# Optimization experiments

Measured on AMD Instinct MI355X. Metric: run time of the kernel, lower is better.

Reference implementation:

```python
import jax, jax.numpy as jnp
import numpy as np

N_NODES = 50000
MAX_NODES = 50000
POS_DIM = 64
IN_DIM = 128
HID = 64
N_LAYERS = 3
BN_EPS = 1e-5


def sinusoidal_encoding(max_len, d_model):
    position = jnp.arange(max_len, dtype=jnp.float32)[:, None]
    div_term = jnp.exp(jnp.arange(0, d_model, 2, dtype=jnp.float32) * (-np.log(10000.0) / d_model))
    ang = position * div_term  # [max_len, d_model//2]
    # interleave sin (even cols) and cos (odd cols)
    return jnp.stack([jnp.sin(ang), jnp.cos(ang)], axis=-1).reshape(max_len, d_model)


def batch_norm(h, gamma, beta):
    mean = jnp.mean(h, axis=0)
    var = jnp.mean(jnp.square(h - mean), axis=0)  # biased, as torch BN training
    return (h - mean) * jax.lax.rsqrt(var + BN_EPS) * gamma + beta


def gcn_conv(h, W, b, row, col, ew, n):
    # PyG GCNConv: h' = D^-1/2 (A + I) D^-1/2 (h W) + b, self-loop weight 1
    hw = h @ W  # [N, HID]
    deg = jnp.zeros((n,), h.dtype).at[col].add(ew) + 1.0  # +1 for self loop
    dinv = jax.lax.rsqrt(deg)
    norm = dinv[row] * ew * dinv[col]  # [E]
    agg = jax.ops.segment_sum(norm[:, None] * hw[row], col, num_segments=n)
    agg = agg + (dinv * dinv)[:, None] * hw  # self-loop term
    return agg + b


def setup_inputs():
    key = jax.random.key(0)
    ks = jax.random.split(key, 16)
    E = 800000
    inp = {
        'x': jax.random.normal(ks[0], (N_NODES, IN_DIM), dtype=jnp.float32),
        'edge_index': jax.random.randint(ks[1], (2, E), 0, N_NODES, dtype=jnp.int32),
        'edge_weight': jax.random.uniform(ks[2], (E,), dtype=jnp.float32),
        'positions': jnp.arange(N_NODES, dtype=jnp.int32),
        'ft_W': jax.random.normal(ks[3], (IN_DIM + POS_DIM, HID), dtype=jnp.float32) * 0.05,
        'ft_b': jnp.zeros((HID,), jnp.float32),
        'ft_gamma': jnp.ones((HID,), jnp.float32),
        'ft_beta': jnp.zeros((HID,), jnp.float32),
        'conv_W': jax.random.normal(ks[4], (N_LAYERS, HID, HID), dtype=jnp.float32) * 0.1,
        'conv_b': jnp.zeros((N_LAYERS, HID), jnp.float32),
        'bn_gamma': jnp.ones((N_LAYERS, HID), jnp.float32),
        'bn_beta': jnp.zeros((N_LAYERS, HID), jnp.float32),
        'out_W1': jax.random.normal(ks[5], (HID, HID // 2), dtype=jnp.float32) * 0.1,
        'out_b1': jnp.zeros((HID // 2,), jnp.float32),
        'out_W2': jax.random.normal(ks[6], (HID // 2, 1), dtype=jnp.float32) * 0.1,
        'out_b2': jnp.zeros((1,), jnp.float32),
    }
    return inp


def reference(x, edge_index, edge_weight, positions, ft_W, ft_b, ft_gamma, ft_beta,
              conv_W, conv_b, bn_gamma, bn_beta, out_W1, out_b1, out_W2, out_b2):
    n = x.shape[0]
    row, col = edge_index[0], edge_index[1]
    pe = sinusoidal_encoding(MAX_NODES, POS_DIM)
    h = jnp.concatenate([x, pe[positions]], axis=1)
    # feature_transform: Linear -> BN -> ReLU (dropout = identity in eval)
    h = jax.nn.relu(batch_norm(h @ ft_W + ft_b, ft_gamma, ft_beta))
    for i in range(N_LAYERS):
        identity = h
        h = gcn_conv(h, conv_W[i], conv_b[i], row, col, edge_weight, n)
        h = jax.nn.relu(batch_norm(h, bn_gamma[i], bn_beta[i]))
        h = h + identity
    h = jax.nn.relu(h @ out_W1 + out_b1)
    out = h @ out_W2 + out_b2  # [N, 1]
    return out.squeeze()
```

## Files before the change

### kernel.cpp

```cpp
#include <hip/hip_runtime.h>
#include <hip/hip_fp16.h>
#include <math.h>

#define HID 64
#define IN_DIM 128
#define POS_DIM 64
#define FT_IN 192
#define BN_EPS 1e-5f
#define PAD 68
#define MAXDEG 64

static inline size_t align256(size_t x){ return (x + 255) & ~(size_t)255; }


__global__ void k_init(unsigned long long* bins, float* statsAll, int N){
  int i = blockIdx.x*blockDim.x + threadIdx.x;
  if (i < N) bins[i] = 0ULL;
  if (i < 512) statsAll[i] = 0.f;
}

__global__ void k_build(const int* __restrict__ row, const int* __restrict__ col,
                        const float* __restrict__ ew,
                        unsigned long long* bins, unsigned* wedges, int E){
  int e = blockIdx.x*blockDim.x + threadIdx.x;
  if (e < E){
    int r = row[e], c = col[e];
    float w = ew[e];
    unsigned long long v = (1ULL<<40)
        | (unsigned long long)(unsigned)__float2uint_rn(w*16777216.0f);
    unsigned long long old = atomicAdd(&bins[c], v);
    unsigned q = (unsigned)(old >> 40);
    if (q < MAXDEG){
      __half hw16 = __float2half(w);
      wedges[(size_t)c*MAXDEG + q] =
          (unsigned)r | ((unsigned)*(unsigned short*)&hw16 << 16);
    }
  }
}

__global__ void k_dinv(const unsigned long long* __restrict__ bins,
                       float* dinv, int N){
  int i = blockIdx.x*blockDim.x + threadIdx.x;
  if (i < N){
    float deg = (float)(bins[i] & 0xFFFFFFFFFFULL) * 5.9604645e-8f;
    dinv[i] = rsqrtf(deg + 1.0f);
  }
}


#define MICRO_FMA(a, b, acc)                                   \
  acc[0].x = fmaf(a.x, b.x, acc[0].x);                         \
  acc[0].y = fmaf(a.x, b.y, acc[0].y);                         \
  acc[0].z = fmaf(a.x, b.z, acc[0].z);                         \
  acc[0].w = fmaf(a.x, b.w, acc[0].w);                         \
  acc[1].x = fmaf(a.y, b.x, acc[1].x);                         \
  acc[1].y = fmaf(a.y, b.y, acc[1].y);                         \
  acc[1].z = fmaf(a.y, b.z, acc[1].z);                         \
  acc[1].w = fmaf(a.y, b.w, acc[1].w);                         \
  acc[2].x = fmaf(a.z, b.x, acc[2].x);                         \
  acc[2].y = fmaf(a.z, b.y, acc[2].y);                         \
  acc[2].z = fmaf(a.z, b.z, acc[2].z);                         \
  acc[2].w = fmaf(a.z, b.w, acc[2].w);                         \
  acc[3].x = fmaf(a.w, b.x, acc[3].x);                         \
  acc[3].y = fmaf(a.w, b.y, acc[3].y);                         \
  acc[3].z = fmaf(a.w, b.z, acc[3].z);                         \
  acc[3].w = fmaf(a.w, b.w, acc[3].w);

__global__ __launch_bounds__(256) void k_h0(
    const float* __restrict__ x, const int* __restrict__ positions,
    const float* __restrict__ ftW, float* __restrict__ h0, float* stats, int N)
{
  __shared__ __align__(16) float Xs[32*PAD];
  __shared__ __align__(16) float Wc[32*64];
  __shared__ float redS[16*64];
  __shared__ float redQ[16*64];
  int tx = threadIdx.x;
  int n0 = blockIdx.x * 64;
  int c4 = (tx & 15) * 4;
  int r4 = (tx >> 4) * 4;
  float4 acc[4];
  acc[0] = acc[1] = acc[2] = acc[3] = make_float4(0.f,0.f,0.f,0.f);

  for (int kc = 0; kc < 6; ++kc){
    #pragma unroll
    for (int i = 0; i < 8; ++i)
      Wc[tx + i*256] = ftW[kc*2048 + tx + i*256];
    if (kc < 4){
      #pragma unroll
      for (int i = 0; i < 2; ++i){
        int s = tx + i*256;
        int row = s >> 3, kk = (s & 7) * 4;
        float4 v = make_float4(0.f,0.f,0.f,0.f);
        int n = n0 + row;
        if (n < N) v = *(const float4*)&x[(size_t)n*IN_DIM + kc*32 + kk];
        Xs[(kk+0)*PAD + row] = v.x;
        Xs[(kk+1)*PAD + row] = v.y;
        Xs[(kk+2)*PAD + row] = v.z;
        Xs[(kk+3)*PAD + row] = v.w;
      }
    } else {
      #pragma unroll
      for (int i = 0; i < 4; ++i){
        int s = tx + i*256;
        int m = s & 63, jj = s >> 6;
        int j = (kc-4)*16 + jj;
        int n = n0 + m;
        float sv = 0.f, cv = 0.f;
        if (n < N){
          float ang = (float)positions[n] * expf((float)(2*j) * -0.14391157f);
          sv = __sinf(ang); cv = __cosf(ang);
        }
        Xs[(2*jj+0)*PAD + m] = sv;
        Xs[(2*jj+1)*PAD + m] = cv;
      }
    }
    __syncthreads();
    #pragma unroll 8
    for (int k = 0; k < 32; ++k){
      float4 a = *(const float4*)(Xs + k*PAD + r4);
      float4 b = *(const float4*)(Wc + k*64 + c4);
      MICRO_FMA(a, b, acc);
    }
    __syncthreads();
  }

  float cs[4] = {0,0,0,0}, cq[4] = {0,0,0,0};
  #pragma unroll
  for (int i = 0; i < 4; ++i){
    int n = n0 + r4 + i;
    if (n < N) *(float4*)&h0[(size_t)n*HID + c4] = acc[i];
    float4 v = (n < N) ? acc[i] : make_float4(0,0,0,0);
    cs[0] += v.x; cs[1] += v.y; cs[2] += v.z; cs[3] += v.w;
    cq[0] += v.x*v.x; cq[1] += v.y*v.y; cq[2] += v.z*v.z; cq[3] += v.w*v.w;
  }
  int g = tx >> 4;
  #pragma unroll
  for (int j = 0; j < 4; ++j){
    redS[g*64 + c4 + j] = cs[j];
    redQ[g*64 + c4 + j] = cq[j];
  }
  __syncthreads();
  if (tx < 64){
    float s = 0.f, q = 0.f;
    #pragma unroll
    for (int gg = 0; gg < 16; ++gg){ s += redS[gg*64 + tx]; q += redQ[gg*64 + tx]; }
    atomicAdd(&stats[tx], s);
    atomicAdd(&stats[64+tx], q);
  }
}

__global__ __launch_bounds__(256) void k_layer(
    const float* __restrict__ aggb, const float* __restrict__ stats,
    const float* __restrict__ gamma, const float* __restrict__ beta, float invN,
    float* __restrict__ hbuf, const float* __restrict__ W,
    const float* __restrict__ dinv, __half* __restrict__ hwh, int N, int residual)
{
  __shared__ __align__(16) float Ws[64*64];
  __shared__ __align__(16) float Hs[64*PAD];
  __shared__ float coefS[128];
  int tx = threadIdx.x;
  int n0 = blockIdx.x * 64;
  if (tx < 64){
    float s = stats[tx], s2 = stats[64+tx];
    float mean = s * invN;
    float var = s2 * invN - mean*mean;
    float scale = rsqrtf(var + BN_EPS) * gamma[tx];
    coefS[tx] = scale;
    coefS[64+tx] = beta[tx] - mean*scale;
  }
  #pragma unroll
  for (int i = 0; i < 16; ++i) Ws[tx + i*256] = W[tx + i*256];
  __syncthreads();
  #pragma unroll
  for (int i = 0; i < 4; ++i){
    int s = tx + i*256;
    int row = s >> 4, cc = (s & 15) * 4;
    int n = n0 + row;
    float4 r = make_float4(0.f,0.f,0.f,0.f);
    if (n < N){
      float4 v = *(const float4*)&aggb[(size_t)n*HID + cc];
      r.x = fmaxf(fmaf(v.x, coefS[cc+0], coefS[64+cc+0]), 0.f);
      r.y = fmaxf(fmaf(v.y, coefS[cc+1], coefS[64+cc+1]), 0.f);
      r.z = fmaxf(fmaf(v.z, coefS[cc+2], coefS[64+cc+2]), 0.f);
      r.w = fmaxf(fmaf(v.w, coefS[cc+3], coefS[64+cc+3]), 0.f);
      if (residual){
        float4 o = *(const float4*)&hbuf[(size_t)n*HID + cc];
        r.x += o.x; r.y += o.y; r.z += o.z; r.w += o.w;
      }
      *(float4*)&hbuf[(size_t)n*HID + cc] = r;
    }
    Hs[(cc+0)*PAD + row] = r.x;
    Hs[(cc+1)*PAD + row] = r.y;
    Hs[(cc+2)*PAD + row] = r.z;
    Hs[(cc+3)*PAD + row] = r.w;
  }
  __syncthreads();
  int c4 = (tx & 15) * 4;
  int r4 = (tx >> 4) * 4;
  float4 acc[4];
  acc[0] = acc[1] = acc[2] = acc[3] = make_float4(0.f,0.f,0.f,0.f);
  #pragma unroll 8
  for (int k = 0; k < 64; ++k){
    float4 a = *(const float4*)(Hs + k*PAD + r4);
    float4 b = *(const float4*)(Ws + k*64 + c4);
    MICRO_FMA(a, b, acc);
  }
  #pragma unroll
  for (int i = 0; i < 4; ++i){
    int n = n0 + r4 + i;
    if (n < N){
      float dn = dinv[n];
      __half2 h01 = __floats2half2_rn(dn*acc[i].x, dn*acc[i].y);
      __half2 h23 = __floats2half2_rn(dn*acc[i].z, dn*acc[i].w);
      *(__half2*)&hwh[(size_t)n*HID + c4]     = h01;
      *(__half2*)&hwh[(size_t)n*HID + c4 + 2] = h23;
    }
  }
}

__global__ __launch_bounds__(256) void k_agg(
    const __half* __restrict__ hwh, const unsigned long long* __restrict__ bins,
    const unsigned* __restrict__ wedges, const float* __restrict__ dinv,
    float* __restrict__ agg, float* stats, int N)
{
  __shared__ float red[512];
  int tx = threadIdx.x;
  int k = tx & 63, w = tx >> 6;
  int n0 = blockIdx.x * 16;
  float ssum = 0.f, ssq = 0.f;
  for (int it = 0; it < 4; ++it){
    int n = n0 + w*4 + it;
    if (n < N){
      int cnt = (int)(bins[n] >> 40);
      if (cnt > MAXDEG) cnt = MAXDEG;
      float acc0 = __half2float(hwh[(size_t)n*HID + k]);
      float acc1 = 0.f, acc2 = 0.f, acc3 = 0.f;
      float acc4 = 0.f, acc5 = 0.f, acc6 = 0.f, acc7 = 0.f;
      unsigned md = (k < cnt) ? wedges[(size_t)n*MAXDEG + k] : 0u;
      int j = 0;
      #define EDGE(T, ACC) {                                              \
        unsigned m_ = __shfl(md, j + T, 64);                              \
        unsigned short eh_ = (unsigned short)(m_ >> 16);                  \
        float ww_ = __half2float(*(__half*)&eh_);                         \
        float g_ = __half2float(hwh[(size_t)(m_ & 0xFFFFu)*HID + k]);     \
        ACC = fmaf(ww_, g_, ACC); }
      for (; j + 8 <= cnt; j += 8){
        EDGE(0, acc0) EDGE(1, acc1) EDGE(2, acc2) EDGE(3, acc3)
        EDGE(4, acc4) EDGE(5, acc5) EDGE(6, acc6) EDGE(7, acc7)
      }
      for (; j < cnt; ++j){ EDGE(0, acc0) }
      #undef EDGE
      float total = ((acc0 + acc1) + (acc2 + acc3))
                  + ((acc4 + acc5) + (acc6 + acc7));
      total *= dinv[n];
      agg[(size_t)n*HID + k] = total;
      ssum += total; ssq += total*total;
    }
  }
  red[tx] = ssum; red[256+tx] = ssq;
  __syncthreads();
  if (tx < 64){
    float s  = red[tx]     + red[64+tx]  + red[128+tx] + red[192+tx];
    float s2 = red[256+tx] + red[320+tx] + red[384+tx] + red[448+tx];
    atomicAdd(&stats[tx], s);
    atomicAdd(&stats[64+tx], s2);
  }
}

__global__ __launch_bounds__(256) void k_out(
    const float* __restrict__ aggb, const float* __restrict__ stats,
    const float* __restrict__ gamma, const float* __restrict__ beta, float invN,
    const float* __restrict__ hbuf,
    const float* __restrict__ W1, const float* __restrict__ b1,
    const float* __restrict__ W2, const float* __restrict__ b2,
    float* __restrict__ out, int N)
{
  __shared__ __align__(16) float Hs[64*PAD];
  __shared__ float red[256];
  __shared__ float coefS[128];
  int tx = threadIdx.x;
  int n0 = blockIdx.x * 64;
  if (tx < 64){
    float s = stats[tx], s2 = stats[64+tx];
    float mean = s * invN;
    float var = s2 * invN - mean*mean;
    float scale = rsqrtf(var + BN_EPS) * gamma[tx];
    coefS[tx] = scale;
    coefS[64+tx] = beta[tx] - mean*scale;
  }
  __syncthreads();
  #pragma unroll
  for (int i = 0; i < 4; ++i){
    int s = tx + i*256;
    int row = s >> 4, cc = (s & 15) * 4;
    int n = n0 + row;
    float4 r = make_float4(0.f,0.f,0.f,0.f);
    if (n < N){
      float4 v = *(const float4*)&aggb[(size_t)n*HID + cc];
      r.x = fmaxf(fmaf(v.x, coefS[cc+0], coefS[64+cc+0]), 0.f);
      r.y = fmaxf(fmaf(v.y, coefS[cc+1], coefS[64+cc+1]), 0.f);
      r.z = fmaxf(fmaf(v.z, coefS[cc+2], coefS[64+cc+2]), 0.f);
      r.w = fmaxf(fmaf(v.w, coefS[cc+3], coefS[64+cc+3]), 0.f);
      float4 o = *(const float4*)&hbuf[(size_t)n*HID + cc];
      r.x += o.x; r.y += o.y; r.z += o.z; r.w += o.w;
    }
    Hs[(cc+0)*PAD + row] = r.x;
    Hs[(cc+1)*PAD + row] = r.y;
    Hs[(cc+2)*PAD + row] = r.z;
    Hs[(cc+3)*PAD + row] = r.w;
  }
  __syncthreads();
  int m = tx & 63, w = tx >> 6, j0 = w*8;
  float acc[8] = {0,0,0,0,0,0,0,0};
  #pragma unroll 8
  for (int k = 0; k < 64; ++k){
    float hv = Hs[k*PAD + m];
    #pragma unroll
    for (int j = 0; j < 8; ++j)
      acc[j] = fmaf(hv, W1[k*32 + j0 + j], acc[j]);
  }
  float part = 0.f;
  #pragma unroll
  for (int j = 0; j < 8; ++j)
    part += fmaxf(acc[j] + b1[j0+j], 0.f) * W2[j0+j];
  red[w*64 + m] = part;
  __syncthreads();
  if (tx < 64){
    int n = n0 + tx;
    if (n < N) out[n] = red[tx] + red[64+tx] + red[128+tx] + red[192+tx] + b2[0];
  }
}

extern "C" void kernel_launch(void* const* d_in, const int* in_sizes, int n_in,
                              void* d_out, int out_size, void* d_ws, size_t ws_size,
                              hipStream_t stream)
{
  const float* x         = (const float*)d_in[0];
  const int*   ei        = (const int*)d_in[1];
  const float* ew        = (const float*)d_in[2];
  const int*   positions = (const int*)d_in[3];
  const float* ftW       = (const float*)d_in[4];
  const float* ft_gamma  = (const float*)d_in[6];
  const float* ft_beta   = (const float*)d_in[7];
  const float* convW     = (const float*)d_in[8];
  const float* bn_gamma  = (const float*)d_in[10];
  const float* bn_beta   = (const float*)d_in[11];
  const float* outW1     = (const float*)d_in[12];
  const float* outb1     = (const float*)d_in[13];
  const float* outW2     = (const float*)d_in[14];
  const float* outb2     = (const float*)d_in[15];
  float* out = (float*)d_out;

  int N = in_sizes[0] / IN_DIM;
  int E = in_sizes[1] / 2;
  const int* row  = ei;
  const int* colv = ei + E;

  char* p = (char*)d_ws;
  auto alloc = [&](size_t bytes){ char* r = p; p += align256(bytes); return r; };
  unsigned long long* bins = (unsigned long long*)alloc((size_t)N*8);
  float*    dinv   = (float*)alloc((size_t)N*4);
  unsigned* wedges = (unsigned*)alloc((size_t)N*MAXDEG*4);
  __half*   hwh    = (__half*)alloc((size_t)N*HID*2);
  float*    aggb   = (float*)alloc((size_t)N*HID*4);
  float*    hbuf   = (float*)alloc((size_t)N*HID*4);
  float*    statsAll = (float*)alloc(512*4);

  float* stats0 = statsAll;
  float* stats1 = statsAll + 128;
  float* stats2 = statsAll + 256;
  float* stats3 = statsAll + 384;

  int nb_n  = (N+255)/256;
  int nb_e  = (E+255)/256;
  int nb64  = (N+63)/64;
  int nb16  = (N+15)/16;
  float invN = 1.0f/(float)N;

  k_init <<<nb_n,256,0,stream>>>(bins,statsAll,N);
  k_build<<<nb_e,256,0,stream>>>(row,colv,ew,bins,wedges,E);
  k_dinv <<<nb_n,256,0,stream>>>(bins,dinv,N);

  k_h0  <<<nb64,256,0,stream>>>(x,positions,ftW,aggb,stats0,N);

  float* statsIn[4] = {stats0, stats1, stats2, stats3};
  for (int i = 0; i < 3; ++i){
    const float* g = (i==0) ? ft_gamma : bn_gamma + (size_t)(i-1)*HID;
    const float* b = (i==0) ? ft_beta  : bn_beta  + (size_t)(i-1)*HID;
    k_layer<<<nb64,256,0,stream>>>(aggb,statsIn[i],g,b,invN,hbuf,
                                   convW + (size_t)i*HID*HID,dinv,hwh,N,(i>0)?1:0);
    k_agg  <<<nb16,256,0,stream>>>(hwh,bins,wedges,dinv,aggb,statsIn[i+1],N);
  }

  k_out<<<nb64,256,0,stream>>>(aggb,stats3,bn_gamma+2*HID,bn_beta+2*HID,invN,
                               hbuf,outW1,outb1,outW2,outb2,out,N);
}
```

Baseline: 437.7 us.

## Split fp16 features into column halves and aggregate each half separately

The transformed features are now stored as two separate N×32 half-precision arrays instead of one N×64 array, and the aggregation runs twice, once per half. Each 32-lane half-wavefront processes its own node. The intent is to shrink each gather pass's working set (3.2MB per half) so it fits better in cache and random neighbor gathers hit more often. The cost is reading the edge lists twice and launching an extra kernel per layer. Edge-list loads and output stores are marked nontemporal.

```diff
diff --git a/kernel.cpp b/kernel.cpp
--- a/kernel.cpp
+++ b/kernel.cpp
@@ -153,7 +153,8 @@
     const float* __restrict__ aggb, const float* __restrict__ stats,
     const float* __restrict__ gamma, const float* __restrict__ beta, float invN,
     float* __restrict__ hbuf, const float* __restrict__ W,
-    const float* __restrict__ dinv, __half* __restrict__ hwh, int N, int residual)
+    const float* __restrict__ dinv, __half* __restrict__ hwhA,
+    __half* __restrict__ hwhB, int N, int residual)
 {
   __shared__ __align__(16) float Ws[64*64];
   __shared__ __align__(16) float Hs[64*PAD];
@@ -212,58 +213,81 @@
       float dn = dinv[n];
       __half2 h01 = __floats2half2_rn(dn*acc[i].x, dn*acc[i].y);
       __half2 h23 = __floats2half2_rn(dn*acc[i].z, dn*acc[i].w);
-      *(__half2*)&hwh[(size_t)n*HID + c4]     = h01;
-      *(__half2*)&hwh[(size_t)n*HID + c4 + 2] = h23;
-    }
-  }
-}
-
-__global__ __launch_bounds__(256) void k_agg(
-    const __half* __restrict__ hwh, const unsigned long long* __restrict__ bins,
+      __half* dst = (c4 < 32) ? (hwhA + (size_t)n*32 + c4)
+                              : (hwhB + (size_t)n*32 + (c4 - 32));
+      *(__half2*)&dst[0] = h01;
+      *(__half2*)&dst[2] = h23;
+    }
+  }
+}
+
+__global__ __launch_bounds__(256) void k_aggH(
+    const __half* __restrict__ hwhH, const unsigned long long* __restrict__ bins,
     const unsigned* __restrict__ wedges, const float* __restrict__ dinv,
-    float* __restrict__ agg, float* stats, int N)
+    float* __restrict__ agg, float* stats, int N, int halfOff)
 {
-  __shared__ float red[512];
+  __shared__ float redS[8*32];
+  __shared__ float redQ[8*32];
   int tx = threadIdx.x;
-  int k = tx & 63, w = tx >> 6;
-  int n0 = blockIdx.x * 16;
-  float ssum = 0.f, ssq = 0.f;
-  for (int it = 0; it < 4; ++it){
-    int n = n0 + w*4 + it;
-    if (n < N){
-      int cnt = (int)(bins[n] >> 40);
-      if (cnt > MAXDEG) cnt = MAXDEG;
-      float acc0 = __half2float(hwh[(size_t)n*HID + k]);
-      float acc1 = 0.f, acc2 = 0.f, acc3 = 0.f;
-      float acc4 = 0.f, acc5 = 0.f, acc6 = 0.f, acc7 = 0.f;
-      unsigned md = (k < cnt) ? wedges[(size_t)n*MAXDEG + k] : 0u;
-      int j = 0;
-      #define EDGE(T, ACC) {                                              \
-        unsigned m_ = __shfl(md, j + T, 64);                              \
-        unsigned short eh_ = (unsigned short)(m_ >> 16);                  \
-        float ww_ = __half2float(*(__half*)&eh_);                         \
-        float g_ = __half2float(hwh[(size_t)(m_ & 0xFFFFu)*HID + k]);     \
-        ACC = fmaf(ww_, g_, ACC); }
-      for (; j + 8 <= cnt; j += 8){
-        EDGE(0, acc0) EDGE(1, acc1) EDGE(2, acc2) EDGE(3, acc3)
-        EDGE(4, acc4) EDGE(5, acc5) EDGE(6, acc6) EDGE(7, acc7)
+  int lane = tx & 63, w = tx >> 6;
+  int hs = lane >> 5;
+  int k = lane & 31;
+  float csum = 0.f, csq = 0.f;
+  int nbase = blockIdx.x*16 + w*4;
+  for (int it = 0; it < 2; ++it){
+    int n = nbase + it*2 + hs;
+    bool act = (n < N);
+    int nn = act ? n : 0;
+    int cnt = act ? (int)(bins[nn] >> 40) : 0;
+    if (cnt > MAXDEG) cnt = MAXDEG;
+    unsigned md0 = (k < cnt)
+        ? __builtin_nontemporal_load(&wedges[(size_t)nn*MAXDEG + k]) : 0u;
+    unsigned md1 = (32 + k < cnt)
+        ? __builtin_nontemporal_load(&wedges[(size_t)nn*MAXDEG + 32 + k]) : 0u;
+    int cm = cnt;
+    cm = max(cm, __shfl_xor(cm, 32, 64));
+    float a0 = act ? __half2float(hwhH[(size_t)nn*32 + k]) : 0.f;
+    float a1=0.f, a2=0.f, a3=0.f, a4=0.f, a5=0.f, a6=0.f, a7=0.f;
+    #define EDGE(MD, T, ACC) {                                            \
+      unsigned m_ = __shfl(MD, (hs<<5) + j + T, 64);                      \
+      unsigned short eh_ = (unsigned short)(m_ >> 16);                    \
+      float ww_ = __half2float(*(__half*)&eh_);                           \
+      float g_ = __half2float(hwhH[(size_t)(m_ & 0xFFFFu)*32 + k]);       \
+      ACC = fmaf(ww_, g_, ACC); }
+    int c0 = min(cm, 32);
+    int j = 0;
+    for (; j + 8 <= c0; j += 8){
+      EDGE(md0,0,a0) EDGE(md0,1,a1) EDGE(md0,2,a2) EDGE(md0,3,a3)
+      EDGE(md0,4,a4) EDGE(md0,5,a5) EDGE(md0,6,a6) EDGE(md0,7,a7)
+    }
+    for (; j < c0; ++j){ EDGE(md0,0,a0) }
+    if (cm > 32){
+      int c1 = cm - 32;
+      j = 0;
+      for (; j + 8 <= c1; j += 8){
+        EDGE(md1,0,a0) EDGE(md1,1,a1) EDGE(md1,2,a2) EDGE(md1,3,a3)
+        EDGE(md1,4,a4) EDGE(md1,5,a5) EDGE(md1,6,a6) EDGE(md1,7,a7)
       }
-      for (; j < cnt; ++j){ EDGE(0, acc0) }
-      #undef EDGE
-      float total = ((acc0 + acc1) + (acc2 + acc3))
-                  + ((acc4 + acc5) + (acc6 + acc7));
-      total *= dinv[n];
-      agg[(size_t)n*HID + k] = total;
-      ssum += total; ssq += total*total;
-    }
-  }
-  red[tx] = ssum; red[256+tx] = ssq;
-  __syncthreads();
-  if (tx < 64){
-    float s  = red[tx]     + red[64+tx]  + red[128+tx] + red[192+tx];
-    float s2 = red[256+tx] + red[320+tx] + red[384+tx] + red[448+tx];
-    atomicAdd(&stats[tx], s);
-    atomicAdd(&stats[64+tx], s2);
+      for (; j < c1; ++j){ EDGE(md1,0,a0) }
+    }
+    #undef EDGE
+    float total = ((a0 + a1) + (a2 + a3)) + ((a4 + a5) + (a6 + a7));
+    if (act){
+      total *= dinv[nn];
+      __builtin_nontemporal_store(total, &agg[(size_t)nn*HID + halfOff + k]);
+      csum += total; csq += total*total;
+    }
+  }
+  int r = w*2 + hs;
+  redS[r*32 + k] = csum;
+  redQ[r*32 + k] = csq;
+  __syncthreads();
+  if (tx < 32){
+    float s = 0.f, q = 0.f;
+    #pragma unroll
+    for (int rr = 0; rr < 8; ++rr){ s += redS[rr*32 + tx]; q += redQ[rr*32 + tx]; }
+    atomicAdd(&stats[halfOff + tx], s);
+    atomicAdd(&stats[64 + halfOff + tx], q);
   }
 }
 
@@ -361,7 +385,8 @@
   unsigned long long* bins = (unsigned long long*)alloc((size_t)N*8);
   float*    dinv   = (float*)alloc((size_t)N*4);
   unsigned* wedges = (unsigned*)alloc((size_t)N*MAXDEG*4);
-  __half*   hwh    = (__half*)alloc((size_t)N*HID*2);
+  __half*   hwhA   = (__half*)alloc((size_t)N*32*2);
+  __half*   hwhB   = (__half*)alloc((size_t)N*32*2);
   float*    aggb   = (float*)alloc((size_t)N*HID*4);
   float*    hbuf   = (float*)alloc((size_t)N*HID*4);
   float*    statsAll = (float*)alloc(512*4);
@@ -388,8 +413,9 @@
     const float* g = (i==0) ? ft_gamma : bn_gamma + (size_t)(i-1)*HID;
     const float* b = (i==0) ? ft_beta  : bn_beta  + (size_t)(i-1)*HID;
     k_layer<<<nb64,256,0,stream>>>(aggb,statsIn[i],g,b,invN,hbuf,
-                                   convW + (size_t)i*HID*HID,dinv,hwh,N,(i>0)?1:0);
-    k_agg  <<<nb16,256,0,stream>>>(hwh,bins,wedges,dinv,aggb,statsIn[i+1],N);
+                                   convW + (size_t)i*HID*HID,dinv,hwhA,hwhB,N,(i>0)?1:0);
+    k_aggH <<<nb16,256,0,stream>>>(hwhA,bins,wedges,dinv,aggb,statsIn[i+1],N,0);
+    k_aggH <<<nb16,256,0,stream>>>(hwhB,bins,wedges,dinv,aggb,statsIn[i+1],N,32);
   }
 
   k_out<<<nb64,256,0,stream>>>(aggb,stats3,bn_gamma+2*HID,bn_beta+2*HID,invN,
```

New measurement: 462.0 us. 5.6% more time.
